# Optimization experiments

Hardware: AMD Instinct MI355X
Metric: run time of the kernel (lower is better)

The kernel has to match this reference:

```python
import jax, jax.numpy as jnp
import numpy as np

B, N, IN_F, OUT_F, H, NUM_EDGE_TYPES = 16, 512, 256, 256, 8, 50
HEAD_DIM = OUT_F // H
LN_EPS = 1e-5


def setup_inputs() -> dict:
    key = jax.random.key(0)
    ks = jax.random.split(key, 8)
    x = jax.random.normal(ks[0], (B, N, IN_F), dtype=jnp.float32)
    adj = jax.random.randint(ks[1], (B, N, N), 0, 2, dtype=jnp.int32)
    edge_types = jax.random.randint(ks[2], (B, N, N), 0, NUM_EDGE_TYPES, dtype=jnp.int32)
    # Parameters (torch Linear stores weight as [out, in]; we keep [in, out] for x @ W)
    W = jax.random.normal(ks[3], (IN_F, OUT_F), dtype=jnp.float32) / np.sqrt(IN_F)
    a1 = jax.random.normal(ks[4], (HEAD_DIM,), dtype=jnp.float32) / np.sqrt(HEAD_DIM)
    a2 = jax.random.normal(ks[5], (HEAD_DIM,), dtype=jnp.float32) / np.sqrt(HEAD_DIM)
    edge_emb = jax.random.normal(ks[6], (NUM_EDGE_TYPES, H), dtype=jnp.float32) * 0.02
    edge_emb = edge_emb.at[0].set(0.0)  # padding_idx=0
    ln_gamma = jnp.ones((OUT_F,), dtype=jnp.float32)
    ln_beta = jnp.zeros((OUT_F,), dtype=jnp.float32)
    return {"x": x, "adj": adj, "edge_types": edge_types, "W": W, "a1": a1,
            "a2": a2, "edge_emb": edge_emb, "ln_gamma": ln_gamma, "ln_beta": ln_beta}


def reference(x, adj, edge_types, W, a1, a2, edge_emb, ln_gamma, ln_beta):
    Bx, Nx, _ = x.shape
    # Wh: [B, N, H, D]
    Wh = (x @ W).reshape(Bx, Nx, H, HEAD_DIM)
    # per-node attention scalars: [B, N, H]
    s1 = jnp.einsum('bnhd,d->bnh', Wh, a1)
    s2 = jnp.einsum('bnhd,d->bnh', Wh, a2)
    # e: [B, N(i), N(j), H]
    e = s1[:, :, None, :] + s2[:, None, :, :] + edge_emb[edge_types]
    e = jnp.where(e > 0, e, 0.2 * e)  # leaky_relu(0.2)
    e = jnp.where((adj == 0)[..., None], jnp.float32(-1e9), e)
    alpha = jax.nn.softmax(e, axis=2)  # softmax over j
    # (dropout omitted: eval mode / deterministic reference)
    h = jnp.einsum('bijh,bjhd->bihd', alpha, Wh).reshape(Bx, Nx, OUT_F)
    # LayerNorm over last dim
    mu = jnp.mean(h, axis=-1, keepdims=True)
    var = jnp.mean(jnp.square(h - mu), axis=-1, keepdims=True)
    hn = (h - mu) * jax.lax.rsqrt(var + LN_EPS) * ln_gamma + ln_beta
    return jax.nn.elu(hn)
```

## Files before the change

kernel.cpp:

```cpp
#include <hip/hip_runtime.h>
#include <hip/hip_bf16.h>
#include <stdint.h>

namespace gat {
constexpr int NB   = 16;
constexpr int NN   = 512;
constexpr int FIN  = 256;
constexpr int FOUT = 256;
constexpr int H    = 8;
constexpr int NE   = 50;
constexpr float L2E  = 1.4426950408889634f;
constexpr float MASK = -115.41500f;
}
using namespace gat;

typedef __attribute__((ext_vector_type(8))) short short8;
typedef __attribute__((ext_vector_type(4))) float f32x4;

__device__ __forceinline__ unsigned pk_bf16(unsigned ulo, unsigned uhi) {
  return __builtin_amdgcn_perm(uhi, ulo, 0x07060302u);
}
__device__ __forceinline__ unsigned pk2f(float a, float b) {
  return pk_bf16(__float_as_uint(a) + 0x8000u, __float_as_uint(b) + 0x8000u);
}

__global__ __launch_bounds__(256) void k_prep(const float* __restrict__ Wm,
                                              unsigned short* __restrict__ WbT) {
  const int k = blockIdx.x;
  const int f = threadIdx.x;
  const unsigned u = __float_as_uint(Wm[k * FOUT + f]) + 0x8000u;
  WbT[f * FIN + k] = (unsigned short)(u >> 16);
}

__global__ __launch_bounds__(512, 4) void k_gemm(
    const float* __restrict__ x, const unsigned short* __restrict__ WbT,
    const float* __restrict__ a1, const float* __restrict__ a2,
    unsigned short* __restrict__ WhT, float* __restrict__ s1, float* __restrict__ s2T)
{
  __shared__ alignas(16) unsigned short xS[16 * 264];
  __shared__ float redG[256 * 18];
  const int t    = threadIdx.x;
  const int row0 = blockIdx.x * 16;

  {
    const int r  = t >> 5;
    const int kb = (t & 31) * 8;
    const float4* xg = (const float4*)(x + (size_t)(row0 + r) * FIN + kb);
    const float4 v0 = xg[0], v1 = xg[1];
    uint4 o;
    o.x = pk2f(v0.x, v0.y); o.y = pk2f(v0.z, v0.w);
    o.z = pk2f(v1.x, v1.y); o.w = pk2f(v1.z, v1.w);
    *(uint4*)&xS[r * 264 + kb] = o;
  }
  __syncthreads();

  const int W    = t >> 6;
  const int w    = W & 3;
  const int kh   = W >> 2;
  const int L    = t & 63;
  const int nn   = L & 15;
  const int quad = L >> 4;
  const unsigned short* wb = WbT + (size_t)(w * 64 + nn) * FIN + kh * 128 + quad * 8;
  const unsigned short* xp = &xS[nn * 264 + kh * 128 + quad * 8];

  f32x4 acc0 = {0.f,0.f,0.f,0.f}, acc1 = {0.f,0.f,0.f,0.f};
  f32x4 acc2 = {0.f,0.f,0.f,0.f}, acc3 = {0.f,0.f,0.f,0.f};

  #pragma unroll
  for (int kc = 0; kc < 4; ++kc) {
    const int k0 = kc * 32;
    const short8 A  = *(const short8*)(xp + k0);
    const short8 B0 = *(const short8*)(wb + k0);
    const short8 B1 = *(const short8*)(wb + 16 * FIN + k0);
    const short8 B2 = *(const short8*)(wb + 32 * FIN + k0);
    const short8 B3 = *(const short8*)(wb + 48 * FIN + k0);
    acc0 = __builtin_amdgcn_mfma_f32_16x16x32_bf16(A, B0, acc0, 0, 0, 0);
    acc1 = __builtin_amdgcn_mfma_f32_16x16x32_bf16(A, B1, acc1, 0, 0, 0);
    acc2 = __builtin_amdgcn_mfma_f32_16x16x32_bf16(A, B2, acc2, 0, 0, 0);
    acc3 = __builtin_amdgcn_mfma_f32_16x16x32_bf16(A, B3, acc3, 0, 0, 0);
  }

  const int tt = (w << 6) | L;
  if (kh == 1) {
    float* rp = redG + tt * 18;
    #pragma unroll
    for (int r = 0; r < 4; ++r) {
      ((float2*)rp)[r]     = {acc0[r * 2 & 3], 0.f};
    }
    rp[0]=acc0[0]; rp[1]=acc0[1]; rp[2]=acc0[2]; rp[3]=acc0[3];
    rp[4]=acc1[0]; rp[5]=acc1[1]; rp[6]=acc1[2]; rp[7]=acc1[3];
    rp[8]=acc2[0]; rp[9]=acc2[1]; rp[10]=acc2[2]; rp[11]=acc2[3];
    rp[12]=acc3[0]; rp[13]=acc3[1]; rp[14]=acc3[2]; rp[15]=acc3[3];
  }
  __syncthreads();
  if (kh == 1) return;

  {
    const float* rp = redG + tt * 18;
    acc0[0]+=rp[0]; acc0[1]+=rp[1]; acc0[2]+=rp[2]; acc0[3]+=rp[3];
    acc1[0]+=rp[4]; acc1[1]+=rp[5]; acc1[2]+=rp[6]; acc1[3]+=rp[7];
    acc2[0]+=rp[8]; acc2[1]+=rp[9]; acc2[2]+=rp[10]; acc2[3]+=rp[11];
    acc3[0]+=rp[12]; acc3[1]+=rp[13]; acc3[2]+=rp[14]; acc3[3]+=rp[15];
  }

  const int b     = row0 >> 9;
  const int node0 = (row0 & 511) + quad * 4;
  f32x4 accs[4] = {acc0, acc1, acc2, acc3};

  #pragma unroll
  for (int ft = 0; ft < 4; ++ft) {
    const int f = w * 64 + ft * 16 + nn;
    uint2 o;
    o.x = pk2f(accs[ft][0], accs[ft][1]);
    o.y = pk2f(accs[ft][2], accs[ft][3]);
    *(uint2*)(WhT + (size_t)((b * 8 + (f >> 5)) * 32 + (f & 31)) * 512 + node0) = o;
  }

  const float a1lo = a1[nn], a1hi = a1[16 + nn];
  const float a2lo = a2[nn], a2hi = a2[16 + nn];
  #pragma unroll
  for (int hh = 0; hh < 2; ++hh) {
    const int h = w * 2 + hh;
    const f32x4 e0 = accs[hh * 2], e1 = accs[hh * 2 + 1];
    float p1[4], p2[4];
    #pragma unroll
    for (int r = 0; r < 4; ++r) {
      p1[r] = e0[r] * a1lo + e1[r] * a1hi;
      p2[r] = e0[r] * a2lo + e1[r] * a2hi;
    }
    #pragma unroll
    for (int r = 0; r < 4; ++r) {
      p1[r] += __shfl_xor(p1[r], 1); p2[r] += __shfl_xor(p2[r], 1);
      p1[r] += __shfl_xor(p1[r], 2); p2[r] += __shfl_xor(p2[r], 2);
      p1[r] += __shfl_xor(p1[r], 4); p2[r] += __shfl_xor(p2[r], 4);
      p1[r] += __shfl_xor(p1[r], 8); p2[r] += __shfl_xor(p2[r], 8);
    }
    if (nn == 0) {
      float4 sv; sv.x = p2[0] * L2E; sv.y = p2[1] * L2E; sv.z = p2[2] * L2E; sv.w = p2[3] * L2E;
      *(float4*)(s2T + (size_t)(b * 8 + h) * 512 + node0) = sv;
      #pragma unroll
      for (int r = 0; r < 4; ++r)
        s1[(size_t)(row0 + quad * 4 + r) * H + h] = p1[r] * L2E;
    }
  }
}

__global__ __launch_bounds__(512, 4) void k_attn(
    const int* __restrict__ adj, const int* __restrict__ ety,
    const float* __restrict__ s1, const float* __restrict__ s2T,
    const unsigned short* __restrict__ WhT, const float* __restrict__ emb,
    const float* __restrict__ gam, const float* __restrict__ bet,
    float* __restrict__ out)
{
  __shared__ float2 embS[4 * 64];
  __shared__ float2 lnS[16 * 4];
  __shared__ float  redS[256 * 18];

  const int t    = threadIdx.x;
  const int b    = blockIdx.x >> 5;
  const int i0   = (blockIdx.x & 31) * 16;
  const int W    = t >> 6;
  const int w    = W & 3;
  const int jh   = W >> 2;
  const int L    = t & 63;
  const int i    = L & 15;
  const int quad = L >> 4;
  const int h0   = w, h1 = w + 4;

  if (t < 256) {
    const int wp = t >> 6, e = t & 63;
    if (e < NE) {
      float2 v; v.x = emb[e * H + wp] * L2E; v.y = emb[e * H + wp + 4] * L2E;
      embS[t] = v;
    }
  }

  const int row = b * NN + i0 + i;
  const float si0 = s1[(size_t)row * H + h0];
  const float si1 = s1[(size_t)row * H + h1];
  const int adjBase = row * NN;
  const int jbase   = jh * 256;
  const float* s2h0 = s2T + (size_t)(b * 8 + h0) * 512;
  const float* s2h1 = s2T + (size_t)(b * 8 + h1) * 512;
  const unsigned short* wt00 = WhT + (size_t)((b * 8 + h0) * 32 + i)      * 512;
  const unsigned short* wt01 = WhT + (size_t)((b * 8 + h0) * 32 + 16 + i) * 512;
  const unsigned short* wt10 = WhT + (size_t)((b * 8 + h1) * 32 + i)      * 512;
  const unsigned short* wt11 = WhT + (size_t)((b * 8 + h1) * 32 + 16 + i) * 512;

  f32x4 acc00 = {0.f,0.f,0.f,0.f}, acc01 = {0.f,0.f,0.f,0.f};
  f32x4 acc10 = {0.f,0.f,0.f,0.f}, acc11 = {0.f,0.f,0.f,0.f};
  float l0 = 0.f, l1 = 0.f;

  __syncthreads();

  #pragma unroll 2
  for (int kc = 0; kc < 8; ++kc) {
    const int ja = jbase + kc * 32 + quad * 8;
    const int4 av0 = *(const int4*)(adj + adjBase + ja);
    const int4 av1 = *(const int4*)(adj + adjBase + ja + 4);
    const int4 ev0 = *(const int4*)(ety + adjBase + ja);
    const int4 ev1 = *(const int4*)(ety + adjBase + ja + 4);
    const float4 sa0 = *(const float4*)(s2h0 + ja);
    const float4 sb0 = *(const float4*)(s2h0 + ja + 4);
    const float4 sa1 = *(const float4*)(s2h1 + ja);
    const float4 sb1 = *(const float4*)(s2h1 + ja + 4);
    const short8 A00 = *(const short8*)(wt00 + ja);
    const short8 A01 = *(const short8*)(wt01 + ja);
    const short8 A10 = *(const short8*)(wt10 + ja);
    const short8 A11 = *(const short8*)(wt11 + ja);

    const int aq[8] = {av0.x, av0.y, av0.z, av0.w, av1.x, av1.y, av1.z, av1.w};
    const int eq[8] = {ev0.x, ev0.y, ev0.z, ev0.w, ev1.x, ev1.y, ev1.z, ev1.w};
    const float s20[8] = {sa0.x, sa0.y, sa0.z, sa0.w, sb0.x, sb0.y, sb0.z, sb0.w};
    const float s21[8] = {sa1.x, sa1.y, sa1.z, sa1.w, sb1.x, sb1.y, sb1.z, sb1.w};

    unsigned u0[8], u1[8];
    #pragma unroll
    for (int q = 0; q < 8; ++q) {
      const float2 em = embS[w * 64 + eq[q]];
      const bool on = (aq[q] != 0);
      float e0 = si0 + s20[q] + em.x;
      float e1 = si1 + s21[q] + em.y;
      e0 = fmaxf(e0, 0.2f * e0);
      e1 = fmaxf(e1, 0.2f * e1);
      e0 = on ? e0 : MASK;
      e1 = on ? e1 : MASK;
      const float p0 = exp2f(e0);
      const float p1 = exp2f(e1);
      l0 += p0; l1 += p1;
      u0[q] = __float_as_uint(p0) + 0x8000u;
      u1[q] = __float_as_uint(p1) + 0x8000u;
    }
    uint4 U0, U1;
    U0.x = pk_bf16(u0[0], u0[1]); U0.y = pk_bf16(u0[2], u0[3]);
    U0.z = pk_bf16(u0[4], u0[5]); U0.w = pk_bf16(u0[6], u0[7]);
    U1.x = pk_bf16(u1[0], u1[1]); U1.y = pk_bf16(u1[2], u1[3]);
    U1.z = pk_bf16(u1[4], u1[5]); U1.w = pk_bf16(u1[6], u1[7]);
    const short8 B0 = __builtin_bit_cast(short8, U0);
    const short8 B1 = __builtin_bit_cast(short8, U1);

    acc00 = __builtin_amdgcn_mfma_f32_16x16x32_bf16(A00, B0, acc00, 0, 0, 0);
    acc01 = __builtin_amdgcn_mfma_f32_16x16x32_bf16(A01, B0, acc01, 0, 0, 0);
    acc10 = __builtin_amdgcn_mfma_f32_16x16x32_bf16(A10, B1, acc10, 0, 0, 0);
    acc11 = __builtin_amdgcn_mfma_f32_16x16x32_bf16(A11, B1, acc11, 0, 0, 0);
  }

  l0 += __shfl_xor(l0, 16); l0 += __shfl_xor(l0, 32);
  l1 += __shfl_xor(l1, 16); l1 += __shfl_xor(l1, 32);

  const int tt = (w << 6) | L;
  if (jh == 1) {
    float* rp = redS + tt * 18;
    rp[0]=acc00[0]; rp[1]=acc00[1]; rp[2]=acc00[2]; rp[3]=acc00[3];
    rp[4]=acc01[0]; rp[5]=acc01[1]; rp[6]=acc01[2]; rp[7]=acc01[3];
    rp[8]=acc10[0]; rp[9]=acc10[1]; rp[10]=acc10[2]; rp[11]=acc10[3];
    rp[12]=acc11[0]; rp[13]=acc11[1]; rp[14]=acc11[2]; rp[15]=acc11[3];
    rp[16]=l0; rp[17]=l1;
  }
  __syncthreads();

  float vals[16]; float mu, rstd;
  if (jh == 0) {
    const float* rp = redS + tt * 18;
    acc00[0]+=rp[0]; acc00[1]+=rp[1]; acc00[2]+=rp[2]; acc00[3]+=rp[3];
    acc01[0]+=rp[4]; acc01[1]+=rp[5]; acc01[2]+=rp[6]; acc01[3]+=rp[7];
    acc10[0]+=rp[8]; acc10[1]+=rp[9]; acc10[2]+=rp[10]; acc10[3]+=rp[11];
    acc11[0]+=rp[12]; acc11[1]+=rp[13]; acc11[2]+=rp[14]; acc11[3]+=rp[15];
    l0 += rp[16]; l1 += rp[17];
    const float inv0 = __builtin_amdgcn_rcpf(l0);
    const float inv1 = __builtin_amdgcn_rcpf(l1);
    #pragma unroll
    for (int r = 0; r < 4; ++r) {
      vals[r]      = acc00[r] * inv0;
      vals[4 + r]  = acc01[r] * inv0;
      vals[8 + r]  = acc10[r] * inv1;
      vals[12 + r] = acc11[r] * inv1;
    }
    float s = 0.f, ss = 0.f;
    #pragma unroll
    for (int k = 0; k < 16; ++k) { s += vals[k]; ss += vals[k] * vals[k]; }
    s += __shfl_xor(s, 16); ss += __shfl_xor(ss, 16);
    s += __shfl_xor(s, 32); ss += __shfl_xor(ss, 32);
    if (quad == 0) { float2 v; v.x = s; v.y = ss; lnS[i * 4 + w] = v; }
  }
  __syncthreads();
  if (jh == 1) return;

  {
    float S = 0.f, SS = 0.f;
    #pragma unroll
    for (int ww = 0; ww < 4; ++ww) { const float2 v = lnS[i * 4 + ww]; S += v.x; SS += v.y; }
    mu = S * (1.0f / 256.0f);
    const float var = SS * (1.0f / 256.0f) - mu * mu;
    rstd = rsqrtf(var + 1e-5f);
  }

  const int fb[4] = { h0 * 32 + quad * 4, h0 * 32 + 16 + quad * 4,
                      h1 * 32 + quad * 4, h1 * 32 + 16 + quad * 4 };
  #pragma unroll
  for (int g = 0; g < 4; ++g) {
    const float4 gv = *(const float4*)(gam + fb[g]);
    const float4 bv = *(const float4*)(bet + fb[g]);
    float4 o;
    o.x = (vals[g*4+0] - mu) * rstd * gv.x + bv.x;
    o.y = (vals[g*4+1] - mu) * rstd * gv.y + bv.y;
    o.z = (vals[g*4+2] - mu) * rstd * gv.z + bv.z;
    o.w = (vals[g*4+3] - mu) * rstd * gv.w + bv.w;
    o.x = o.x > 0.f ? o.x : exp2f(o.x * L2E) - 1.f;
    o.y = o.y > 0.f ? o.y : exp2f(o.y * L2E) - 1.f;
    o.z = o.z > 0.f ? o.z : exp2f(o.z * L2E) - 1.f;
    o.w = o.w > 0.f ? o.w : exp2f(o.w * L2E) - 1.f;
    *(float4*)(out + (size_t)row * FOUT + fb[g]) = o;
  }
}

extern "C" void kernel_launch(void* const* d_in, const int* in_sizes, int n_in,
                              void* d_out, int out_size, void* d_ws, size_t ws_size,
                              hipStream_t stream) {
  (void)in_sizes; (void)n_in; (void)out_size; (void)ws_size;
  const float* x   = (const float*)d_in[0];
  const int*   adj = (const int*)  d_in[1];
  const int*   ety = (const int*)  d_in[2];
  const float* Wm  = (const float*)d_in[3];
  const float* a1  = (const float*)d_in[4];
  const float* a2  = (const float*)d_in[5];
  const float* emb = (const float*)d_in[6];
  const float* gam = (const float*)d_in[7];
  const float* bet = (const float*)d_in[8];
  float* out = (float*)d_out;

  unsigned short* WhT = (unsigned short*)d_ws;
  unsigned short* WbT = WhT + (size_t)NB * H * 32 * 512;
  float* s1  = (float*)(WbT + (size_t)FOUT * FIN);
  float* s2T = s1 + (size_t)NB * NN * H;

  k_prep<<<dim3(FIN),  dim3(256), 0, stream>>>(Wm, WbT);
  k_gemm<<<dim3(NB * NN / 16), dim3(512), 0, stream>>>(x, WbT, a1, a2, WhT, s1, s2T);
  k_attn<<<dim3(NB * (NN / 16)), dim3(512), 0, stream>>>(adj, ety, s1, s2T, WhT, emb, gam, bet, out);
}
```

Before: 139.4 us.

## Pack adjacency and edge types into byte codes and stage s2 in LDS

A new pre-pass kernel packs each adj/edge_type pair into one byte (type in low 6 bits, edge-present flag in bit 6). The attention kernel then reads 1 byte per pair instead of 8 and preloads all its codes into registers up front. Per-batch s2 scores are staged into shared memory instead of being read from global memory inside the loop. It also drops a dead store loop in the GEMM reduction. The cost is an extra kernel launch and a full pass over adj/ety, plus more LDS and register use in the attention kernel.

```diff
diff --git a/kernel.cpp b/kernel.cpp
--- a/kernel.cpp
+++ b/kernel.cpp
@@ -30,6 +30,26 @@
   const int f = threadIdx.x;
   const unsigned u = __float_as_uint(Wm[k * FOUT + f]) + 0x8000u;
   WbT[f * FIN + k] = (unsigned short)(u >> 16);
+}
+
+__global__ __launch_bounds__(256) void k_pack(const int* __restrict__ adj,
+                                              const int* __restrict__ ety,
+                                              unsigned* __restrict__ codes) {
+  const size_t base = ((size_t)blockIdx.x * 256 + threadIdx.x) * 16;
+  const int4* ap = (const int4*)(adj + base);
+  const int4* ep = (const int4*)(ety + base);
+  unsigned o[4];
+  #pragma unroll
+  for (int g = 0; g < 4; ++g) {
+    const int4 a = ap[g];
+    const int4 e = ep[g];
+    o[g] = (unsigned)(e.x | (a.x << 6))
+         | ((unsigned)(e.y | (a.y << 6)) << 8)
+         | ((unsigned)(e.z | (a.z << 6)) << 16)
+         | ((unsigned)(e.w | (a.w << 6)) << 24);
+  }
+  uint4 v; v.x = o[0]; v.y = o[1]; v.z = o[2]; v.w = o[3];
+  *(uint4*)(codes + base / 4) = v;
 }
 
 __global__ __launch_bounds__(512, 4) void k_gemm(
@@ -83,10 +103,6 @@
   const int tt = (w << 6) | L;
   if (kh == 1) {
     float* rp = redG + tt * 18;
-    #pragma unroll
-    for (int r = 0; r < 4; ++r) {
-      ((float2*)rp)[r]     = {acc0[r * 2 & 3], 0.f};
-    }
     rp[0]=acc0[0]; rp[1]=acc0[1]; rp[2]=acc0[2]; rp[3]=acc0[3];
     rp[4]=acc1[0]; rp[5]=acc1[1]; rp[6]=acc1[2]; rp[7]=acc1[3];
     rp[8]=acc2[0]; rp[9]=acc2[1]; rp[10]=acc2[2]; rp[11]=acc2[3];
@@ -146,7 +162,7 @@
 }
 
 __global__ __launch_bounds__(512, 4) void k_attn(
-    const int* __restrict__ adj, const int* __restrict__ ety,
+    const unsigned char* __restrict__ codes,
     const float* __restrict__ s1, const float* __restrict__ s2T,
     const unsigned short* __restrict__ WhT, const float* __restrict__ emb,
     const float* __restrict__ gam, const float* __restrict__ bet,
@@ -154,6 +170,7 @@
 {
   __shared__ float2 embS[4 * 64];
   __shared__ float2 lnS[16 * 4];
+  __shared__ float  s2S[8 * 512];
   __shared__ float  redS[256 * 18];
 
   const int t    = threadIdx.x;
@@ -167,6 +184,12 @@
   const int quad = L >> 4;
   const int h0   = w, h1 = w + 4;
 
+  {
+    const float4* sg = (const float4*)(s2T + (size_t)b * 8 * 512);
+    float4* ss = (float4*)s2S;
+    ss[t]       = sg[t];
+    ss[t + 512] = sg[t + 512];
+  }
   if (t < 256) {
     const int wp = t >> 6, e = t & 63;
     if (e < NE) {
@@ -175,13 +198,18 @@
     }
   }
 
-  const int row = b * NN + i0 + i;
+  const int row   = b * NN + i0 + i;
+  const int jbase = jh * 256;
+
+  uint2 cw[8];
+  {
+    const unsigned char* cp = codes + (size_t)row * NN + jbase + quad * 8;
+    #pragma unroll
+    for (int kc = 0; kc < 8; ++kc) cw[kc] = *(const uint2*)(cp + kc * 32);
+  }
+
   const float si0 = s1[(size_t)row * H + h0];
   const float si1 = s1[(size_t)row * H + h1];
-  const int adjBase = row * NN;
-  const int jbase   = jh * 256;
-  const float* s2h0 = s2T + (size_t)(b * 8 + h0) * 512;
-  const float* s2h1 = s2T + (size_t)(b * 8 + h1) * 512;
   const unsigned short* wt00 = WhT + (size_t)((b * 8 + h0) * 32 + i)      * 512;
   const unsigned short* wt01 = WhT + (size_t)((b * 8 + h0) * 32 + 16 + i) * 512;
   const unsigned short* wt10 = WhT + (size_t)((b * 8 + h1) * 32 + i)      * 512;
@@ -196,29 +224,25 @@
   #pragma unroll 2
   for (int kc = 0; kc < 8; ++kc) {
     const int ja = jbase + kc * 32 + quad * 8;
-    const int4 av0 = *(const int4*)(adj + adjBase + ja);
-    const int4 av1 = *(const int4*)(adj + adjBase + ja + 4);
-    const int4 ev0 = *(const int4*)(ety + adjBase + ja);
-    const int4 ev1 = *(const int4*)(ety + adjBase + ja + 4);
-    const float4 sa0 = *(const float4*)(s2h0 + ja);
-    const float4 sb0 = *(const float4*)(s2h0 + ja + 4);
-    const float4 sa1 = *(const float4*)(s2h1 + ja);
-    const float4 sb1 = *(const float4*)(s2h1 + ja + 4);
     const short8 A00 = *(const short8*)(wt00 + ja);
     const short8 A01 = *(const short8*)(wt01 + ja);
     const short8 A10 = *(const short8*)(wt10 + ja);
     const short8 A11 = *(const short8*)(wt11 + ja);
-
-    const int aq[8] = {av0.x, av0.y, av0.z, av0.w, av1.x, av1.y, av1.z, av1.w};
-    const int eq[8] = {ev0.x, ev0.y, ev0.z, ev0.w, ev1.x, ev1.y, ev1.z, ev1.w};
+    const float4 sa0 = *(const float4*)&s2S[h0 * 512 + ja];
+    const float4 sb0 = *(const float4*)&s2S[h0 * 512 + ja + 4];
+    const float4 sa1 = *(const float4*)&s2S[h1 * 512 + ja];
+    const float4 sb1 = *(const float4*)&s2S[h1 * 512 + ja + 4];
+
     const float s20[8] = {sa0.x, sa0.y, sa0.z, sa0.w, sb0.x, sb0.y, sb0.z, sb0.w};
     const float s21[8] = {sa1.x, sa1.y, sa1.z, sa1.w, sb1.x, sb1.y, sb1.z, sb1.w};
 
     unsigned u0[8], u1[8];
     #pragma unroll
     for (int q = 0; q < 8; ++q) {
-      const float2 em = embS[w * 64 + eq[q]];
-      const bool on = (aq[q] != 0);
+      const unsigned cword = (q < 4) ? cw[kc].x : cw[kc].y;
+      const unsigned c = (cword >> ((q & 3) * 8)) & 0x7fu;
+      const bool on = c >= 64u;
+      const float2 em = embS[w * 64 + (c & 63u)];
       float e0 = si0 + s20[q] + em.x;
       float e1 = si1 + s21[q] + em.y;
       e0 = fmaxf(e0, 0.2f * e0);
@@ -331,10 +355,12 @@
 
   unsigned short* WhT = (unsigned short*)d_ws;
   unsigned short* WbT = WhT + (size_t)NB * H * 32 * 512;
-  float* s1  = (float*)(WbT + (size_t)FOUT * FIN);
-  float* s2T = s1 + (size_t)NB * NN * H;
+  float* s1   = (float*)(WbT + (size_t)FOUT * FIN);
+  float* s2T  = s1 + (size_t)NB * NN * H;
+  unsigned char* codes = (unsigned char*)(s2T + (size_t)NB * H * NN);
 
   k_prep<<<dim3(FIN),  dim3(256), 0, stream>>>(Wm, WbT);
+  k_pack<<<dim3(NB * NN * NN / (256 * 16)), dim3(256), 0, stream>>>(adj, ety, (unsigned*)codes);
   k_gemm<<<dim3(NB * NN / 16), dim3(512), 0, stream>>>(x, WbT, a1, a2, WhT, s1, s2T);
-  k_attn<<<dim3(NB * (NN / 16)), dim3(512), 0, stream>>>(adj, ety, s1, s2T, WhT, emb, gam, bet, out);
-}
+  k_attn<<<dim3(NB * (NN / 16)), dim3(512), 0, stream>>>(codes, s1, s2T, WhT, emb, gam, bet, out);
+}
```

Result: no change. 138.6 us (-0.6%).
